# Optimization experiments

Measured on AMD Instinct MI355X. Metric: run time of the kernel, lower is better.

The kernel has to match this reference:

```python
import jax, jax.numpy as jnp
import numpy as np

B, D_IN, D_H, D_BOT, D_EXP, N_CLS = 8192, 1024, 2048, 512, 1024, 10


def _w(key, shape):
    return jax.random.normal(key, shape, dtype=jnp.float32) * 0.02


def setup_inputs() -> dict:
    key = jax.random.key(0)
    ks = jax.random.split(key, 16)
    return {
        "x": jax.random.normal(ks[0], (B, D_IN), dtype=jnp.float32),
        "labels": jax.random.randint(ks[1], (B,), 0, N_CLS, dtype=jnp.int32),
        # encoder: 1024 -> 2048 -> 512 (ReLU after each)
        "W1": _w(ks[2], (D_IN, D_H)), "b1": jnp.zeros((D_H,), jnp.float32),
        "W2": _w(ks[3], (D_H, D_BOT)), "b2": jnp.zeros((D_BOT,), jnp.float32),
        # per-class expert MLPs (identical shapes, stacked): 512 -> 1024 -> 512, ReLU after each
        "EW1": _w(ks[4], (N_CLS, D_BOT, D_EXP)), "Eb1": jnp.zeros((N_CLS, D_EXP), jnp.float32),
        "EW2": _w(ks[5], (N_CLS, D_EXP, D_BOT)), "Eb2": jnp.zeros((N_CLS, D_BOT), jnp.float32),
        # decoder: 512 -> 2048 (ReLU) -> 1024 (no final activation)
        "DW1": _w(ks[6], (D_BOT, D_H)), "Db1": jnp.zeros((D_H,), jnp.float32),
        "DW2": _w(ks[7], (D_H, D_IN)), "Db2": jnp.zeros((D_IN,), jnp.float32),
    }


def reference(x, labels, W1, b1, W2, b2, EW1, Eb1, EW2, Eb2, DW1, Db1, DW2, Db2):
    # encoder
    h = jax.nn.relu(x @ W1 + b1)           # [B, 2048]
    h = jax.nn.relu(h @ W2 + b2)           # [B, 512]
    # class-routed experts: compute all experts densely, then gather by label
    he = jax.nn.relu(jnp.einsum('bi,eio->beo', h, EW1) + Eb1[None])   # [B, E, 1024]
    he = jax.nn.relu(jnp.einsum('beh,eho->beo', he, EW2) + Eb2[None]) # [B, E, 512]
    sel = jnp.take_along_axis(he, labels[:, None, None].astype(jnp.int32), axis=1)[:, 0]  # [B, 512]
    # decoder (activation after first layer only)
    d = jax.nn.relu(sel @ DW1 + Db1)       # [B, 2048]
    out = d @ DW2 + Db2                    # [B, 1024]
    return out
```

## Files before the change

kernel.cpp:

```cpp
#include <hip/hip_runtime.h>
#include <hip/hip_bf16.h>
#include <stdint.h>

typedef __attribute__((ext_vector_type(8))) short bf16x8;
typedef __attribute__((ext_vector_type(4))) float f32x4;

__device__ __forceinline__ unsigned short f2bf(float f) {
  unsigned int u = __float_as_uint(f);
  u += 0x7fff + ((u >> 16) & 1);
  return (unsigned short)(u >> 16);
}

__device__ __forceinline__ void gload16(const void* g, void* l) {
  __builtin_amdgcn_global_load_lds(
      (const __attribute__((address_space(1))) void*)g,
      (__attribute__((address_space(3))) void*)l, 16, 0, 0);
}

#define Bsz   8192
#define D_IN  1024
#define D_H   2048
#define D_BOT 512
#define D_EXP 1024
#define N_CLS 10

__global__ __launch_bounds__(256) void k_prep_all(
    const float* __restrict__ W1,  const float* __restrict__ W2,
    const float* __restrict__ EW1, const float* __restrict__ EW2,
    const float* __restrict__ DW1, const float* __restrict__ DW2,
    unsigned short* __restrict__ W1T,  unsigned short* __restrict__ W2T,
    unsigned short* __restrict__ EW1T, unsigned short* __restrict__ EW2T,
    unsigned short* __restrict__ DW1T, unsigned short* __restrict__ DW2T,
    const float* __restrict__ x, unsigned short* __restrict__ xb,
    const int* __restrict__ lab, int* __restrict__ counts,
    int* __restrict__ starts, int* __restrict__ perm) {
  const int bid = blockIdx.x;
  const int tx = threadIdx.x, ty = threadIdx.y;
  const int t = ty * 32 + tx;

  if (bid < 16384) {
    const float* in; unsigned short* out; int K, N, tile;
    if (bid < 2048)        { in = W1;  out = W1T;  K = D_IN;  N = D_H;   tile = bid; }
    else if (bid < 3072)   { in = W2;  out = W2T;  K = D_H;   N = D_BOT; tile = bid - 2048; }
    else if (bid < 8192)   { int r = bid - 3072; int e = r >> 9; tile = r & 511;
                             K = D_BOT; N = D_EXP;
                             in = EW1 + (size_t)e * K * N; out = EW1T + (size_t)e * K * N; }
    else if (bid < 13312)  { int r = bid - 8192; int e = r >> 9; tile = r & 511;
                             K = D_EXP; N = D_BOT;
                             in = EW2 + (size_t)e * K * N; out = EW2T + (size_t)e * K * N; }
    else if (bid < 14336)  { in = DW1; out = DW1T; K = D_BOT; N = D_H;   tile = bid - 13312; }
    else                   { in = DW2; out = DW2T; K = D_H;   N = D_IN;  tile = bid - 14336; }
    const int ntx = N >> 5;
    const int n0 = (tile % ntx) * 32, k0 = (tile / ntx) * 32;

    __shared__ float tl[32][33];
#pragma unroll
    for (int i = 0; i < 4; ++i) {
      int k = ty + i * 8;
      tl[k][tx] = in[(size_t)(k0 + k) * N + n0 + tx];
    }
    __syncthreads();
#pragma unroll
    for (int i = 0; i < 4; ++i) {
      int n = ty + i * 8;
      out[(size_t)(n0 + n) * K + k0 + tx] = f2bf(tl[tx][n]);
    }
    return;
  }

  if (bid == 16384) {
    __shared__ int scnt[N_CLS], scur[N_CLS];
    if (t < N_CLS) scnt[t] = 0;
    __syncthreads();
    for (int i = 0; i < 32; ++i)
      atomicAdd(&scnt[lab[t * 32 + i]], 1);
    __syncthreads();
    if (t == 0) {
      int s = 0;
      for (int e = 0; e < N_CLS; ++e) {
        starts[e] = s; scur[e] = s; counts[e] = scnt[e]; s += scnt[e];
      }
    }
    __syncthreads();
    for (int i = 0; i < 32; ++i) {
      int b = t * 32 + i;
      int p = atomicAdd(&scur[lab[b]], 1);
      perm[p] = b;
    }
    return;
  }

  {
    int i = ((bid - 16385) * 256 + t) * 8;
    const float4* p = (const float4*)(x + i);
    float4 a = p[0], b = p[1];
    uint4 o;
    o.x = (unsigned)f2bf(a.x) | ((unsigned)f2bf(a.y) << 16);
    o.y = (unsigned)f2bf(a.z) | ((unsigned)f2bf(a.w) << 16);
    o.z = (unsigned)f2bf(b.x) | ((unsigned)f2bf(b.y) << 16);
    o.w = (unsigned)f2bf(b.z) | ((unsigned)f2bf(b.w) << 16);
    *(uint4*)(xb + i) = o;
  }
}

template <int BM, int BN, bool RELU, bool BF16OUT>
__global__ __launch_bounds__(512, 2) void k_gemm8(
    const unsigned short* __restrict__ A,
    const unsigned short* __restrict__ WT,
    const float* __restrict__ bias,
    void* __restrict__ Cv,
    int M, int N, int K) {
  constexpr int WROWS = BM / 2;
  constexpr int QR = WROWS / 2;
  constexpr int FMq = QR / 16;
  constexpr int ACH = BM / 64;
  constexpr int BCH = BN / 64;

  const int nby = gridDim.y;
  const int nwg = gridDim.x * nby;
  int orig = blockIdx.x + gridDim.x * blockIdx.y;
  int q = nwg >> 3, r = nwg & 7;
  int xcd = orig & 7, idx = orig >> 3;
  int wg = (xcd < r ? xcd * (q + 1) : r * (q + 1) + (xcd - r) * q) + idx;
  int bx = wg / nby, by = wg % nby;
  const int m0 = bx * BM, n0 = by * BN;

  __shared__ __align__(16) unsigned short As[2][BM * 64];
  __shared__ __align__(16) unsigned short Bs[2][BN * 64];

  const int t = threadIdx.x;
  const int l = t & 63;
  const int w = t >> 6;
  const int wm = w >> 2, wn = w & 3;

  const int rl = t >> 3;
  const int sl16 = (t & 7) ^ (rl & 7);
  const unsigned short* asrc[ACH];
  const unsigned short* bsrc[BCH];
#pragma unroll
  for (int i = 0; i < ACH; ++i)
    asrc[i] = A + (size_t)(m0 + i * 64 + rl) * K + sl16 * 8;
#pragma unroll
  for (int i = 0; i < BCH; ++i)
    bsrc[i] = WT + (size_t)(n0 + i * 64 + rl) * K + sl16 * 8;
  const int dst = t * 8;

  auto STAGE = [&](int kt, int buf) {
#pragma unroll
    for (int i = 0; i < ACH; ++i)
      gload16(asrc[i] + kt * 64, &As[buf][i * 4096 + dst]);
#pragma unroll
    for (int i = 0; i < BCH; ++i)
      gload16(bsrc[i] + kt * 64, &Bs[buf][i * 4096 + dst]);
  };

  f32x4 acc[2][2][FMq][2] = {};
  bf16x8 af[FMq][2];
  bf16x8 bq[2][2][2];

  const int la = l & 15;
  const int ko = l >> 4;
  const int arow0 = wm * WROWS + la;
  const int brow0 = wn * 64 + la;

  const int nt = K / 64;
  STAGE(0, 0);

  for (int kt = 0; kt < nt; ++kt) {
    const int cur = kt & 1;
    const char* Ab = (const char*)As[cur];
    const char* Bb = (const char*)Bs[cur];

    asm volatile("s_waitcnt vmcnt(0)" ::: "memory");
    __builtin_amdgcn_s_barrier();
    if (kt + 1 < nt) STAGE(kt + 1, cur ^ 1);
    __builtin_amdgcn_sched_barrier(0);

#pragma unroll
    for (int fm = 0; fm < FMq; ++fm)
#pragma unroll
      for (int ks = 0; ks < 2; ++ks) {
        int row = arow0 + fm * 16;
        int s = ks * 4 + ko;
        af[fm][ks] = *(const bf16x8*)(Ab + (row << 7) + ((s ^ (row & 7)) << 4));
      }
#pragma unroll
    for (int fn = 0; fn < 2; ++fn)
#pragma unroll
      for (int ks = 0; ks < 2; ++ks) {
        int row = brow0 + fn * 16;
        int s = ks * 4 + ko;
        bq[0][fn][ks] = *(const bf16x8*)(Bb + (row << 7) + ((s ^ (row & 7)) << 4));
      }
    __builtin_amdgcn_s_setprio(1);
#pragma unroll
    for (int fm = 0; fm < FMq; ++fm)
#pragma unroll
      for (int fn = 0; fn < 2; ++fn)
#pragma unroll
        for (int ks = 0; ks < 2; ++ks)
          acc[0][0][fm][fn] = __builtin_amdgcn_mfma_f32_16x16x32_bf16(
              af[fm][ks], bq[0][fn][ks], acc[0][0][fm][fn], 0, 0, 0);
    __builtin_amdgcn_s_setprio(0);
    __builtin_amdgcn_s_barrier();

#pragma unroll
    for (int fn = 0; fn < 2; ++fn)
#pragma unroll
      for (int ks = 0; ks < 2; ++ks) {
        int row = brow0 + 32 + fn * 16;
        int s = ks * 4 + ko;
        bq[1][fn][ks] = *(const bf16x8*)(Bb + (row << 7) + ((s ^ (row & 7)) << 4));
      }
    __builtin_amdgcn_s_setprio(1);
#pragma unroll
    for (int fm = 0; fm < FMq; ++fm)
#pragma unroll
      for (int fn = 0; fn < 2; ++fn)
#pragma unroll
        for (int ks = 0; ks < 2; ++ks)
          acc[0][1][fm][fn] = __builtin_amdgcn_mfma_f32_16x16x32_bf16(
              af[fm][ks], bq[1][fn][ks], acc[0][1][fm][fn], 0, 0, 0);
    __builtin_amdgcn_s_setprio(0);
    __builtin_amdgcn_s_barrier();

#pragma unroll
    for (int fm = 0; fm < FMq; ++fm)
#pragma unroll
      for (int ks = 0; ks < 2; ++ks) {
        int row = arow0 + QR + fm * 16;
        int s = ks * 4 + ko;
        af[fm][ks] = *(const bf16x8*)(Ab + (row << 7) + ((s ^ (row & 7)) << 4));
      }
    __builtin_amdgcn_s_setprio(1);
#pragma unroll
    for (int fm = 0; fm < FMq; ++fm)
#pragma unroll
      for (int fn = 0; fn < 2; ++fn)
#pragma unroll
        for (int ks = 0; ks < 2; ++ks)
          acc[1][0][fm][fn] = __builtin_amdgcn_mfma_f32_16x16x32_bf16(
              af[fm][ks], bq[0][fn][ks], acc[1][0][fm][fn], 0, 0, 0);
    __builtin_amdgcn_s_setprio(0);
    __builtin_amdgcn_s_barrier();

    __builtin_amdgcn_s_setprio(1);
#pragma unroll
    for (int fm = 0; fm < FMq; ++fm)
#pragma unroll
      for (int fn = 0; fn < 2; ++fn)
#pragma unroll
        for (int ks = 0; ks < 2; ++ks)
          acc[1][1][fm][fn] = __builtin_amdgcn_mfma_f32_16x16x32_bf16(
              af[fm][ks], bq[1][fn][ks], acc[1][1][fm][fn], 0, 0, 0);
    __builtin_amdgcn_s_setprio(0);
  }
  asm volatile("s_waitcnt vmcnt(0)" ::: "memory");

  const int crow0 = m0 + wm * WROWS;
  const int ccol0 = n0 + wn * 64;
#pragma unroll
  for (int qn = 0; qn < 2; ++qn)
#pragma unroll
    for (int fn = 0; fn < 2; ++fn) {
      int c = ccol0 + qn * 32 + fn * 16 + la;
      float bv = bias[c];
#pragma unroll
      for (int qm = 0; qm < 2; ++qm)
#pragma unroll
        for (int fm = 0; fm < FMq; ++fm)
#pragma unroll
          for (int j = 0; j < 4; ++j) {
            int rr = crow0 + qm * QR + fm * 16 + (ko << 2) + j;
            float v = acc[qm][qn][fm][fn][j] + bv;
            if (RELU) v = fmaxf(v, 0.0f);
            if (BF16OUT) ((unsigned short*)Cv)[(size_t)rr * N + c] = f2bf(v);
            else         ((float*)Cv)[(size_t)rr * N + c] = v;
          }
    }
}

template <int TBM, int TBN, int WM, int WN,
          bool RELU, bool BF16OUT, bool GROUPED, bool SCATTER, bool GATHER>
__global__ __launch_bounds__(256) void k_gemm(
    const unsigned short* __restrict__ A,
    const unsigned short* __restrict__ WT,
    const float* __restrict__ bias,
    void* __restrict__ Cv,
    int M, int N, int K,
    const int* __restrict__ starts, const int* __restrict__ counts,
    const int* __restrict__ perm) {
  constexpr int FM = TBM / WM / 16;
  constexpr int FN = TBN / WN / 16;
  constexpr int ALOADS = TBM / 64;
  constexpr int BLOADS = TBN / 64;
  constexpr int LDS_LD = ALOADS + BLOADS;

  const int nby = gridDim.y;
  const int nwg = gridDim.x * nby;
  int orig = blockIdx.x + gridDim.x * blockIdx.y;
  int q = nwg >> 3, r = nwg & 7;
  int xcd = orig & 7, idx = orig >> 3;
  int wg = (xcd < r ? xcd * (q + 1) : r * (q + 1) + (xcd - r) * q) + idx;
  int bx = wg / nby, by = wg % nby;

  int Meff, start = 0, mo;
  const unsigned short* Wp = WT;
  const float* biasp = bias;
  if (GROUPED) {
    int bxr = bx;
    int found = 0;
#pragma unroll
    for (int e = 0; e < N_CLS; ++e) {
      int c = counts[e];
      int nb = (c + TBM - 1) / TBM;
      if (!found && bxr < nb) {
        found = 1; Meff = c; start = starts[e]; mo = bxr * TBM;
        Wp = WT + (size_t)e * N * K; biasp = bias + (size_t)e * N;
      }
      if (!found) bxr -= nb;
    }
    if (!found) return;
    if (!GATHER) A += (size_t)start * K;
  } else {
    Meff = M; mo = bx * TBM;
  }
  const int n0 = by * TBN;

  __shared__ __align__(16) unsigned short As[3][TBM * 32];
  __shared__ __align__(16) unsigned short Bs[3][TBN * 32];

  const int t = threadIdx.x;
  const int l = t & 63;
  const int w = t >> 6;
  const int wm = (w / WN) * (TBM / WM);
  const int wn = (w % WN) * (TBN / WN);

  const int srow = t >> 2;
  const int scol = (t & 3) * 8;
  const unsigned short* ag[ALOADS];
  const unsigned short* bg[BLOADS];
#pragma unroll
  for (int i = 0; i < ALOADS; ++i) {
    int arow = mo + srow + i * 64;
    if (GROUPED) arow = arow < Meff ? arow : Meff - 1;
    int srcrow = GATHER ? perm[start + arow] : arow;
    ag[i] = A + (size_t)srcrow * K + scol;
  }
#pragma unroll
  for (int i = 0; i < BLOADS; ++i)
    bg[i] = Wp + (size_t)(n0 + srow + i * 64) * K + scol;

  auto STAGE = [&](int buf) {
#pragma unroll
    for (int i = 0; i < ALOADS; ++i) {
      gload16(ag[i], &As[buf][t * 8 + i * 2048]);
      ag[i] += 32;
    }
#pragma unroll
    for (int i = 0; i < BLOADS; ++i) {
      gload16(bg[i], &Bs[buf][t * 8 + i * 2048]);
      bg[i] += 32;
    }
  };

  f32x4 acc[FM][FN] = {};

  const int nt = K / 32;
  STAGE(0);
  STAGE(1);
  for (int tI = 0; tI < nt; ++tI) {
    if (tI + 1 < nt)
      asm volatile("s_waitcnt vmcnt(%0)" :: "i"(LDS_LD) : "memory");
    else
      asm volatile("s_waitcnt vmcnt(0)" ::: "memory");
    __builtin_amdgcn_s_barrier();
    __builtin_amdgcn_sched_barrier(0);
    if (tI + 2 < nt) STAGE((tI + 2) % 3);

    const int cur = tI % 3;
    bf16x8 af[FM], bfr[FN];
#pragma unroll
    for (int i = 0; i < FM; ++i)
      af[i] = *(const bf16x8*)(&As[cur][(wm + i * 16 + (l & 15)) * 32 + (l >> 4) * 8]);
#pragma unroll
    for (int i = 0; i < FN; ++i)
      bfr[i] = *(const bf16x8*)(&Bs[cur][(wn + i * 16 + (l & 15)) * 32 + (l >> 4) * 8]);
#pragma unroll
    for (int mi = 0; mi < FM; ++mi)
#pragma unroll
      for (int ni = 0; ni < FN; ++ni)
        acc[mi][ni] = __builtin_amdgcn_mfma_f32_16x16x32_bf16(af[mi], bfr[ni], acc[mi][ni], 0, 0, 0);
  }

  const int cb = n0 + wn + (l & 15);
#pragma unroll
  for (int ni = 0; ni < FN; ++ni) {
    int c = cb + ni * 16;
    float bv = biasp[c];
#pragma unroll
    for (int mi = 0; mi < FM; ++mi) {
#pragma unroll
      for (int j = 0; j < 4; ++j) {
        int rl2 = wm + mi * 16 + ((l >> 4) << 2) + j;
        int re = mo + rl2;
        if (GROUPED && re >= Meff) continue;
        float v = acc[mi][ni][j] + bv;
        if (RELU) v = fmaxf(v, 0.0f);
        int orow;
        if (SCATTER)      orow = perm[start + re];
        else if (GROUPED) orow = start + re;
        else              orow = re;
        if (BF16OUT) ((unsigned short*)Cv)[(size_t)orow * N + c] = f2bf(v);
        else         ((float*)Cv)[(size_t)orow * N + c] = v;
      }
    }
  }
}

#define GX_GROUPED 74

extern "C" void kernel_launch(void* const* d_in, const int* in_sizes, int n_in,
                              void* d_out, int out_size, void* d_ws, size_t ws_size,
                              hipStream_t stream) {
  const float* x      = (const float*)d_in[0];
  const int*   labels = (const int*)d_in[1];
  const float* W1  = (const float*)d_in[2];  const float* b1  = (const float*)d_in[3];
  const float* W2  = (const float*)d_in[4];  const float* b2  = (const float*)d_in[5];
  const float* EW1 = (const float*)d_in[6];  const float* Eb1 = (const float*)d_in[7];
  const float* EW2 = (const float*)d_in[8];  const float* Eb2 = (const float*)d_in[9];
  const float* DW1 = (const float*)d_in[10]; const float* Db1 = (const float*)d_in[11];
  const float* DW2 = (const float*)d_in[12]; const float* Db2 = (const float*)d_in[13];
  float* out = (float*)d_out;

  char* ws = (char*)d_ws;
  size_t o = 0;
  unsigned short* W1T  = (unsigned short*)(ws + o); o += (size_t)D_IN * D_H * 2;
  unsigned short* W2T  = (unsigned short*)(ws + o); o += (size_t)D_H * D_BOT * 2;
  unsigned short* EW1T = (unsigned short*)(ws + o); o += (size_t)N_CLS * D_BOT * D_EXP * 2;
  unsigned short* EW2T = (unsigned short*)(ws + o); o += (size_t)N_CLS * D_EXP * D_BOT * 2;
  unsigned short* DW1T = (unsigned short*)(ws + o); o += (size_t)D_BOT * D_H * 2;
  unsigned short* DW2T = (unsigned short*)(ws + o); o += (size_t)D_H * D_IN * 2;
  unsigned short* xb   = (unsigned short*)(ws + o); o += (size_t)Bsz * D_IN * 2;
  unsigned short* e1p  = xb;
  unsigned short* actA = (unsigned short*)(ws + o); o += (size_t)Bsz * D_H * 2;
  unsigned short* h2   = (unsigned short*)(ws + o); o += (size_t)Bsz * D_BOT * 2;
  unsigned short* sel  = (unsigned short*)(ws + o); o += (size_t)Bsz * D_BOT * 2;
  int* counts = (int*)(ws + o);
  int* starts = counts + 16;
  int* perm   = counts + 64;

  k_prep_all<<<16384 + 1 + 4096, dim3(32, 8), 0, stream>>>(
      W1, W2, EW1, EW2, DW1, DW2,
      W1T, W2T, EW1T, EW2T, DW1T, DW2T,
      x, xb, labels, counts, starts, perm);

  k_gemm8<256, 256, true, true><<<dim3(Bsz / 256, D_H / 256), 512, 0, stream>>>(
      xb, W1T, b1, actA, Bsz, D_H, D_IN);
  k_gemm<128, 64, 4, 1, true, true, false, false, false><<<dim3(Bsz / 128, D_BOT / 64), 256, 0, stream>>>(
      actA, W2T, b2, h2, Bsz, D_BOT, D_H, nullptr, nullptr, nullptr);

  k_gemm<128, 128, 2, 2, true, true, true, false, true><<<dim3(GX_GROUPED, D_EXP / 128), 256, 0, stream>>>(
      h2, EW1T, Eb1, e1p, Bsz, D_EXP, D_BOT, starts, counts, perm);
  k_gemm<128, 64, 4, 1, true, true, true, true, false><<<dim3(GX_GROUPED, D_BOT / 64), 256, 0, stream>>>(
      e1p, EW2T, Eb2, sel, Bsz, D_BOT, D_EXP, starts, counts, perm);

  k_gemm8<256, 256, true, true><<<dim3(Bsz / 256, D_H / 256), 512, 0, stream>>>(
      sel, DW1T, Db1, actA, Bsz, D_H, D_BOT);
  k_gemm8<128, 256, false, false><<<dim3(Bsz / 128, D_IN / 256), 512, 0, stream>>>(
      actA, DW2T, Db2, out, Bsz, D_IN, D_H);
}
```

Baseline: 236.9 us.

## Split GEMM LDS into quarter-tile buffers with interleaved prefetch pipeline

Replaces the templated 8-wave GEMM with a fixed 256x256 kernel whose LDS is divided into eight quarter buffers (A/B halves across two stages). Global-to-LDS loads for the next tiles are issued one quarter at a time between MFMA phases, with partial vmcnt waits instead of a full drain each iteration. This is meant to overlap memory traffic with compute more finely. The final decoder GEMM also moves from a 128-row to a 256-row tile, which halves its grid and raises per-block reuse but may hurt load balance. The staggered buffer reuse relies on careful barrier placement to avoid read/write races.

```diff
diff --git a/kernel.cpp b/kernel.cpp
--- a/kernel.cpp
+++ b/kernel.cpp
@@ -103,19 +103,13 @@
   }
 }
 
-template <int BM, int BN, bool RELU, bool BF16OUT>
-__global__ __launch_bounds__(512, 2) void k_gemm8(
+template <bool RELU, bool BF16OUT>
+__global__ __launch_bounds__(512, 2) void k_g256(
     const unsigned short* __restrict__ A,
     const unsigned short* __restrict__ WT,
     const float* __restrict__ bias,
     void* __restrict__ Cv,
     int M, int N, int K) {
-  constexpr int WROWS = BM / 2;
-  constexpr int QR = WROWS / 2;
-  constexpr int FMq = QR / 16;
-  constexpr int ACH = BM / 64;
-  constexpr int BCH = BN / 64;
-
   const int nby = gridDim.y;
   const int nwg = gridDim.x * nby;
   int orig = blockIdx.x + gridDim.x * blockIdx.y;
@@ -123,156 +117,171 @@
   int xcd = orig & 7, idx = orig >> 3;
   int wg = (xcd < r ? xcd * (q + 1) : r * (q + 1) + (xcd - r) * q) + idx;
   int bx = wg / nby, by = wg % nby;
-  const int m0 = bx * BM, n0 = by * BN;
-
-  __shared__ __align__(16) unsigned short As[2][BM * 64];
-  __shared__ __align__(16) unsigned short Bs[2][BN * 64];
+  const int m0 = bx * 256, n0 = by * 256;
+
+  __shared__ __align__(16) unsigned short lds[8][8192];
 
   const int t = threadIdx.x;
   const int l = t & 63;
   const int w = t >> 6;
   const int wm = w >> 2, wn = w & 3;
-
-  const int rl = t >> 3;
-  const int sl16 = (t & 7) ^ (rl & 7);
-  const unsigned short* asrc[ACH];
-  const unsigned short* bsrc[BCH];
-#pragma unroll
-  for (int i = 0; i < ACH; ++i)
-    asrc[i] = A + (size_t)(m0 + i * 64 + rl) * K + sl16 * 8;
-#pragma unroll
-  for (int i = 0; i < BCH; ++i)
-    bsrc[i] = WT + (size_t)(n0 + i * 64 + rl) * K + sl16 * 8;
-  const int dst = t * 8;
-
-  auto STAGE = [&](int kt, int buf) {
-#pragma unroll
-    for (int i = 0; i < ACH; ++i)
-      gload16(asrc[i] + kt * 64, &As[buf][i * 4096 + dst]);
-#pragma unroll
-    for (int i = 0; i < BCH; ++i)
-      gload16(bsrc[i] + kt * 64, &Bs[buf][i * 4096 + dst]);
-  };
-
-  f32x4 acc[2][2][FMq][2] = {};
-  bf16x8 af[FMq][2];
+  const int la = l & 15, ko = l >> 4;
+
+  const int sr = t >> 3;
+  const int c16 = (t & 7) ^ (sr & 7);
+  const unsigned short* pA0  = A  + (size_t)(m0 + sr) * K + c16 * 8;
+  const unsigned short* pA0b = A  + (size_t)(m0 + 64 + sr) * K + c16 * 8;
+  const unsigned short* pA1  = A  + (size_t)(m0 + 128 + sr) * K + c16 * 8;
+  const unsigned short* pA1b = A  + (size_t)(m0 + 192 + sr) * K + c16 * 8;
+  const unsigned short* pB0  = WT + (size_t)(n0 + sr) * K + c16 * 8;
+  const unsigned short* pB0b = WT + (size_t)(n0 + 64 + sr) * K + c16 * 8;
+  const unsigned short* pB1  = WT + (size_t)(n0 + 128 + sr) * K + c16 * 8;
+  const unsigned short* pB1b = WT + (size_t)(n0 + 192 + sr) * K + c16 * 8;
+  const int dlo = t * 8, dhi = 4096 + t * 8;
+
+  const int nt = K / 64;
+
+  gload16(pA0, &lds[0][dlo]);  gload16(pA0b, &lds[0][dhi]);
+  gload16(pB0, &lds[1][dlo]);  gload16(pB0b, &lds[1][dhi]);
+  gload16(pB1, &lds[2][dlo]);  gload16(pB1b, &lds[2][dhi]);
+  gload16(pA1, &lds[3][dlo]);  gload16(pA1b, &lds[3][dhi]);
+  asm volatile("s_waitcnt vmcnt(4)" ::: "memory");
+  gload16(pA0 + 64, &lds[4][dlo]);  gload16(pA0b + 64, &lds[4][dhi]);
+  gload16(pB0 + 64, &lds[5][dlo]);  gload16(pB0b + 64, &lds[5][dhi]);
+  gload16(pB1 + 64, &lds[6][dlo]);  gload16(pB1b + 64, &lds[6][dhi]);
+  asm volatile("s_waitcnt vmcnt(6)" ::: "memory");
+  __builtin_amdgcn_s_barrier();
+
+  f32x4 acc[2][4][2][2] = {};
+  bf16x8 af[4][2];
   bf16x8 bq[2][2][2];
-
-  const int la = l & 15;
-  const int ko = l >> 4;
-  const int arow0 = wm * WROWS + la;
-  const int brow0 = wn * 64 + la;
-
-  const int nt = K / 64;
-  STAGE(0, 0);
 
   for (int kt = 0; kt < nt; ++kt) {
     const int cur = kt & 1;
-    const char* Ab = (const char*)As[cur];
-    const char* Bb = (const char*)Bs[cur];
-
-    asm volatile("s_waitcnt vmcnt(0)" ::: "memory");
-    __builtin_amdgcn_s_barrier();
-    if (kt + 1 < nt) STAGE(kt + 1, cur ^ 1);
+    const int cs = cur * 4;
+    const char* sA0 = (const char*)lds[cs];
+    const char* sB0 = (const char*)lds[cs + 1];
+    const char* sB1 = (const char*)lds[cs + 2];
+    const char* sA1 = (const char*)lds[cs + 3];
+
+#pragma unroll
+    for (int fm = 0; fm < 4; ++fm) {
+      int rr = wm * 64 + fm * 16 + la;
+#pragma unroll
+      for (int ks = 0; ks < 2; ++ks)
+        af[fm][ks] = *(const bf16x8*)(sA0 + (rr << 7) + (((ks * 4 + ko) ^ (rr & 7)) << 4));
+    }
+#pragma unroll
+    for (int fn = 0; fn < 2; ++fn) {
+      int cc = wn * 32 + fn * 16 + la;
+#pragma unroll
+      for (int ks = 0; ks < 2; ++ks)
+        bq[0][fn][ks] = *(const bf16x8*)(sB0 + (cc << 7) + (((ks * 4 + ko) ^ (cc & 7)) << 4));
+    }
+    if (kt + 1 < nt) {
+      int sl = (cur ^ 1) * 4 + 3;
+      gload16(pA1 + (kt + 1) * 64, &lds[sl][dlo]);
+      gload16(pA1b + (kt + 1) * 64, &lds[sl][dhi]);
+    }
     __builtin_amdgcn_sched_barrier(0);
-
-#pragma unroll
-    for (int fm = 0; fm < FMq; ++fm)
-#pragma unroll
-      for (int ks = 0; ks < 2; ++ks) {
-        int row = arow0 + fm * 16;
-        int s = ks * 4 + ko;
-        af[fm][ks] = *(const bf16x8*)(Ab + (row << 7) + ((s ^ (row & 7)) << 4));
-      }
-#pragma unroll
-    for (int fn = 0; fn < 2; ++fn)
-#pragma unroll
-      for (int ks = 0; ks < 2; ++ks) {
-        int row = brow0 + fn * 16;
-        int s = ks * 4 + ko;
-        bq[0][fn][ks] = *(const bf16x8*)(Bb + (row << 7) + ((s ^ (row & 7)) << 4));
-      }
+    __builtin_amdgcn_s_barrier();
     __builtin_amdgcn_s_setprio(1);
 #pragma unroll
-    for (int fm = 0; fm < FMq; ++fm)
+    for (int fm = 0; fm < 4; ++fm)
 #pragma unroll
       for (int fn = 0; fn < 2; ++fn)
 #pragma unroll
         for (int ks = 0; ks < 2; ++ks)
-          acc[0][0][fm][fn] = __builtin_amdgcn_mfma_f32_16x16x32_bf16(
-              af[fm][ks], bq[0][fn][ks], acc[0][0][fm][fn], 0, 0, 0);
+          acc[0][fm][0][fn] = __builtin_amdgcn_mfma_f32_16x16x32_bf16(
+              af[fm][ks], bq[0][fn][ks], acc[0][fm][0][fn], 0, 0, 0);
     __builtin_amdgcn_s_setprio(0);
     __builtin_amdgcn_s_barrier();
 
 #pragma unroll
-    for (int fn = 0; fn < 2; ++fn)
-#pragma unroll
-      for (int ks = 0; ks < 2; ++ks) {
-        int row = brow0 + 32 + fn * 16;
-        int s = ks * 4 + ko;
-        bq[1][fn][ks] = *(const bf16x8*)(Bb + (row << 7) + ((s ^ (row & 7)) << 4));
-      }
+    for (int fn = 0; fn < 2; ++fn) {
+      int cc = wn * 32 + fn * 16 + la;
+#pragma unroll
+      for (int ks = 0; ks < 2; ++ks)
+        bq[1][fn][ks] = *(const bf16x8*)(sB1 + (cc << 7) + (((ks * 4 + ko) ^ (cc & 7)) << 4));
+    }
+    if (kt + 2 < nt) {
+      gload16(pA0 + (kt + 2) * 64, &lds[cs][dlo]);
+      gload16(pA0b + (kt + 2) * 64, &lds[cs][dhi]);
+    }
+    __builtin_amdgcn_sched_barrier(0);
+    __builtin_amdgcn_s_barrier();
     __builtin_amdgcn_s_setprio(1);
 #pragma unroll
-    for (int fm = 0; fm < FMq; ++fm)
+    for (int fm = 0; fm < 4; ++fm)
 #pragma unroll
       for (int fn = 0; fn < 2; ++fn)
 #pragma unroll
         for (int ks = 0; ks < 2; ++ks)
-          acc[0][1][fm][fn] = __builtin_amdgcn_mfma_f32_16x16x32_bf16(
-              af[fm][ks], bq[1][fn][ks], acc[0][1][fm][fn], 0, 0, 0);
+          acc[0][fm][1][fn] = __builtin_amdgcn_mfma_f32_16x16x32_bf16(
+              af[fm][ks], bq[1][fn][ks], acc[0][fm][1][fn], 0, 0, 0);
     __builtin_amdgcn_s_setprio(0);
     __builtin_amdgcn_s_barrier();
 
 #pragma unroll
-    for (int fm = 0; fm < FMq; ++fm)
-#pragma unroll
-      for (int ks = 0; ks < 2; ++ks) {
-        int row = arow0 + QR + fm * 16;
-        int s = ks * 4 + ko;
-        af[fm][ks] = *(const bf16x8*)(Ab + (row << 7) + ((s ^ (row & 7)) << 4));
-      }
+    for (int fm = 0; fm < 4; ++fm) {
+      int rr = wm * 64 + fm * 16 + la;
+#pragma unroll
+      for (int ks = 0; ks < 2; ++ks)
+        af[fm][ks] = *(const bf16x8*)(sA1 + (rr << 7) + (((ks * 4 + ko) ^ (rr & 7)) << 4));
+    }
+    if (kt + 2 < nt) {
+      gload16(pB0 + (kt + 2) * 64, &lds[cs + 1][dlo]);
+      gload16(pB0b + (kt + 2) * 64, &lds[cs + 1][dhi]);
+    }
+    __builtin_amdgcn_sched_barrier(0);
+    __builtin_amdgcn_s_barrier();
     __builtin_amdgcn_s_setprio(1);
 #pragma unroll
-    for (int fm = 0; fm < FMq; ++fm)
+    for (int fm = 0; fm < 4; ++fm)
 #pragma unroll
       for (int fn = 0; fn < 2; ++fn)
 #pragma unroll
         for (int ks = 0; ks < 2; ++ks)
-          acc[1][0][fm][fn] = __builtin_amdgcn_mfma_f32_16x16x32_bf16(
-              af[fm][ks], bq[0][fn][ks], acc[1][0][fm][fn], 0, 0, 0);
+          acc[1][fm][0][fn] = __builtin_amdgcn_mfma_f32_16x16x32_bf16(
+              af[fm][ks], bq[0][fn][ks], acc[1][fm][0][fn], 0, 0, 0);
     __builtin_amdgcn_s_setprio(0);
     __builtin_amdgcn_s_barrier();
 
+    if (kt + 2 < nt) {
+      gload16(pB1 + (kt + 2) * 64, &lds[cs + 2][dlo]);
+      gload16(pB1b + (kt + 2) * 64, &lds[cs + 2][dhi]);
+    }
+    __builtin_amdgcn_sched_barrier(0);
+    __builtin_amdgcn_s_barrier();
     __builtin_amdgcn_s_setprio(1);
 #pragma unroll
-    for (int fm = 0; fm < FMq; ++fm)
+    for (int fm = 0; fm < 4; ++fm)
 #pragma unroll
       for (int fn = 0; fn < 2; ++fn)
 #pragma unroll
         for (int ks = 0; ks < 2; ++ks)
-          acc[1][1][fm][fn] = __builtin_amdgcn_mfma_f32_16x16x32_bf16(
-              af[fm][ks], bq[1][fn][ks], acc[1][1][fm][fn], 0, 0, 0);
+          acc[1][fm][1][fn] = __builtin_amdgcn_mfma_f32_16x16x32_bf16(
+              af[fm][ks], bq[1][fn][ks], acc[1][fm][1][fn], 0, 0, 0);
     __builtin_amdgcn_s_setprio(0);
+    asm volatile("s_waitcnt vmcnt(6)" ::: "memory");
+    __builtin_amdgcn_s_barrier();
   }
   asm volatile("s_waitcnt vmcnt(0)" ::: "memory");
 
-  const int crow0 = m0 + wm * WROWS;
-  const int ccol0 = n0 + wn * 64;
-#pragma unroll
-  for (int qn = 0; qn < 2; ++qn)
+#pragma unroll
+  for (int nh = 0; nh < 2; ++nh)
 #pragma unroll
     for (int fn = 0; fn < 2; ++fn) {
-      int c = ccol0 + qn * 32 + fn * 16 + la;
+      int c = n0 + nh * 128 + wn * 32 + fn * 16 + la;
       float bv = bias[c];
 #pragma unroll
-      for (int qm = 0; qm < 2; ++qm)
-#pragma unroll
-        for (int fm = 0; fm < FMq; ++fm)
-#pragma unroll
-          for (int j = 0; j < 4; ++j) {
-            int rr = crow0 + qm * QR + fm * 16 + (ko << 2) + j;
-            float v = acc[qm][qn][fm][fn][j] + bv;
+      for (int mh = 0; mh < 2; ++mh)
+#pragma unroll
+        for (int fm = 0; fm < 4; ++fm)
+#pragma unroll
+          for (int jj = 0; jj < 4; ++jj) {
+            int rr = m0 + mh * 128 + wm * 64 + fm * 16 + (ko << 2) + jj;
+            float v = acc[mh][fm][nh][fn][jj] + bv;
             if (RELU) v = fmaxf(v, 0.0f);
             if (BF16OUT) ((unsigned short*)Cv)[(size_t)rr * N + c] = f2bf(v);
             else         ((float*)Cv)[(size_t)rr * N + c] = v;
@@ -455,7 +464,7 @@
       W1T, W2T, EW1T, EW2T, DW1T, DW2T,
       x, xb, labels, counts, starts, perm);
 
-  k_gemm8<256, 256, true, true><<<dim3(Bsz / 256, D_H / 256), 512, 0, stream>>>(
+  k_g256<true, true><<<dim3(Bsz / 256, D_H / 256), 512, 0, stream>>>(
       xb, W1T, b1, actA, Bsz, D_H, D_IN);
   k_gemm<128, 64, 4, 1, true, true, false, false, false><<<dim3(Bsz / 128, D_BOT / 64), 256, 0, stream>>>(
       actA, W2T, b2, h2, Bsz, D_BOT, D_H, nullptr, nullptr, nullptr);
@@ -465,8 +474,8 @@
   k_gemm<128, 64, 4, 1, true, true, true, true, false><<<dim3(GX_GROUPED, D_BOT / 64), 256, 0, stream>>>(
       e1p, EW2T, Eb2, sel, Bsz, D_BOT, D_EXP, starts, counts, perm);
 
-  k_gemm8<256, 256, true, true><<<dim3(Bsz / 256, D_H / 256), 512, 0, stream>>>(
+  k_g256<true, true><<<dim3(Bsz / 256, D_H / 256), 512, 0, stream>>>(
       sel, DW1T, Db1, actA, Bsz, D_H, D_BOT);
-  k_gemm8<128, 256, false, false><<<dim3(Bsz / 128, D_IN / 256), 512, 0, stream>>>(
+  k_g256<false, false><<<dim3(Bsz / 256, D_IN / 256), 512, 0, stream>>>(
       actA, DW2T, Db2, out, Bsz, D_IN, D_H);
 }
```

Result: no change. 235.6 us (-0.5%).
